# Performance work log

Hardware: AMD Instinct MI355X
Metric: run time of the kernel (lower is better)

Reference implementation:

```python
import jax, jax.numpy as jnp
import numpy as np

THRESHOLD = 0.5        # correspondence distance threshold (init kwarg)
MAX_ITERS = 50         # fixed iteration count (open3d's max_iteration)
EPS = 1e-6


def setup_inputs() -> dict:
    key = jax.random.key(0)
    k1, k2 = jax.random.split(key)
    B, N, M = 8, 2048, 2048
    source = jax.random.normal(k1, (B, N, 3), dtype=jnp.float32)
    target = jax.random.normal(k2, (B, M, 3), dtype=jnp.float32)
    return {"source": source, "target": target}


def _icp(source, target):
    """Batched point-to-point ICP. source: (B,N,3), target: (B,M,3) -> (B,4,4)."""
    B, N, _ = source.shape
    dt = source.dtype
    t_sq = jnp.sum(target * target, axis=-1)  # (B,M), constant across iterations

    def step(T, _):
        R, tr = T[:, :3, :3], T[:, :3, 3]
        src = jnp.einsum('bij,bnj->bni', R, source) + tr[:, None, :]  # (B,N,3)
        # brute-force nearest neighbor: squared distances (B,N,M)
        d2 = (jnp.sum(src * src, axis=-1)[:, :, None]
              - 2.0 * jnp.einsum('bnd,bmd->bnm', src, target)
              + t_sq[:, None, :])
        idx = jnp.argmin(d2, axis=-1)                                   # (B,N)
        mind2 = jnp.take_along_axis(d2, idx[..., None], axis=-1)[..., 0]
        nn = jnp.take_along_axis(target, idx[..., None], axis=1)        # (B,N,3)
        # inlier mask: correspondences within threshold
        w = (mind2 < THRESHOLD * THRESHOLD).astype(dt)                  # (B,N)
        wsum = jnp.maximum(jnp.sum(w, axis=-1, keepdims=True), EPS)     # (B,1)
        cs = jnp.sum(w[..., None] * src, axis=1) / wsum                 # (B,3)
        ct = jnp.sum(w[..., None] * nn, axis=1) / wsum                  # (B,3)
        Sc = src - cs[:, None, :]
        Tc = nn - ct[:, None, :]
        # cross-covariance H = sum_n w_n (s_n - cs)(t_n - ct)^T  -> (B,3,3)
        H = jnp.einsum('bn,bni,bnj->bij', w, Sc, Tc)
        U, _, Vh = jnp.linalg.svd(H, full_matrices=False)
        V = jnp.swapaxes(Vh, -1, -2)
        # reflection fix (Kabsch): R = V diag(1,1,sign(det(V U^T))) U^T
        d = jnp.sign(jnp.linalg.det(jnp.einsum('bij,bkj->bik', V, U)))
        scale = jnp.stack([jnp.ones_like(d), jnp.ones_like(d), d], axis=-1)
        Rd = jnp.einsum('bij,bj,bkj->bik', V, scale, U)                 # (B,3,3)
        td = ct - jnp.einsum('bij,bj->bi', Rd, cs)                      # (B,3)
        top = jnp.concatenate([Rd, td[:, :, None]], axis=-1)            # (B,3,4)
        bot = jnp.broadcast_to(jnp.array([0., 0., 0., 1.], dtype=dt), (B, 1, 4))
        delta = jnp.concatenate([top, bot], axis=1)                     # (B,4,4)
        return jnp.einsum('bij,bjk->bik', delta, T), None

    T0 = jnp.broadcast_to(jnp.eye(4, dtype=dt), (B, 4, 4))
    Tfin, _ = jax.lax.scan(step, T0, None, length=MAX_ITERS)
    return Tfin


def reference(source, target):
    return _icp(source, target)
```

## Files before the change

kernel.cpp:

```cpp
#include <hip/hip_runtime.h>
#include <stdint.h>

#define BATCH 8
#define NPTS 2048
#define MPTS 2048
#define ITERS 50
#define THR2 0.25f
#define CHUNKS 32
#define SRC_PER_BLOCK 64
#define PTS 8
#define NTHREADS 1024
#define NWAVES 16
#define SLICE_LEN 16

__global__ __launch_bounds__(NTHREADS)
void icp_kernel(const float* __restrict__ src,
                const float* __restrict__ tgt,
                float* __restrict__ out,
                float* __restrict__ ws)
{
    const int tid   = threadIdx.x;
    const int blk   = blockIdx.x;
    const int b     = blk >> 5;
    const int chunk = blk & 31;
    const int g     = tid & 7;
    const int s     = tid >> 3;
    const int lane  = tid & 63;
    const int wv    = tid >> 6;

    __shared__ float4 tgt4[MPTS];
    __shared__ float  red[NWAVES][65];
    __shared__ float  srcP[SRC_PER_BLOCK][3];
    __shared__ float4 bcastT4[3];

    const float* tb = tgt + (size_t)b * MPTS * 3;
    for (int m = tid; m < MPTS; m += NTHREADS) {
        float tx = tb[m*3+0], ty = tb[m*3+1], tz = tb[m*3+2];
        tgt4[m] = make_float4(-2.f*tx, -2.f*ty, -2.f*tz, tx*tx + ty*ty + tz*tz);
    }
    const float* sb = src + (size_t)b * NPTS * 3 + (size_t)chunk * SRC_PER_BLOCK * 3;
    if (tid < SRC_PER_BLOCK) {
        srcP[tid][0] = sb[tid*3+0];
        srcP[tid][1] = sb[tid*3+1];
        srcP[tid][2] = sb[tid*3+2];
    }
    float px[PTS], py[PTS], pz[PTS];
#pragma unroll
    for (int r = 0; r < PTS; ++r) {
        int i = g*PTS + r;
        px[r] = sb[i*3+0]; py[r] = sb[i*3+1]; pz[r] = sb[i*3+2];
    }
    __syncthreads();

    float r00=1.f,r01=0.f,r02=0.f, r10=0.f,r11=1.f,r12=0.f, r20=0.f,r21=0.f,r22=1.f;
    float t0=0.f,t1=0.f,t2=0.f;

    unsigned int* stamp = (unsigned int*)ws;
    float* slots = ws + 512;

    for (int it = 0; it < ITERS; ++it) {
        float sx[PTS], sy[PTS], sz[PTS];
#pragma unroll
        for (int r = 0; r < PTS; ++r) {
            sx[r] = r00*px[r] + r01*py[r] + r02*pz[r] + t0;
            sy[r] = r10*px[r] + r11*py[r] + r12*pz[r] + t1;
            sz[r] = r20*px[r] + r21*py[r] + r22*pz[r] + t2;
        }
        float best[PTS];
#pragma unroll
        for (int r = 0; r < PTS; ++r) best[r] = __int_as_float(0x7F800000);

        const int base = s * SLICE_LEN;
#pragma unroll 8
        for (int i = 0; i < SLICE_LEN; ++i) {
            int jo = (i + s) & (SLICE_LEN - 1);
            int jj = base + jo;
            float4 q = tgt4[jj];
#pragma unroll
            for (int r = 0; r < PTS; ++r) {
                float d = fmaf(sx[r], q.x, fmaf(sy[r], q.y, fmaf(sz[r], q.z, q.w)));
                unsigned int pd = (__float_as_uint(d) & 0xFFFFF800u) | (unsigned int)jj;
                best[r] = fminf(best[r], __uint_as_float(pd));
            }
        }
#pragma unroll
        for (int r = 0; r < PTS; ++r) {
            float v = best[r];
            v = fminf(v, __shfl_xor(v, 8, 64));
            v = fminf(v, __shfl_xor(v, 16, 64));
            v = fminf(v, __shfl_xor(v, 32, 64));
            best[r] = v;
        }
        if (lane < 8) {
#pragma unroll
            for (int r = 0; r < PTS; ++r) red[wv][lane*PTS + r] = best[r];
        }
        __syncthreads();

        if (tid < 64) {
            float m = red[0][tid];
#pragma unroll
            for (int ww = 1; ww < NWAVES; ++ww) m = fminf(m, red[ww][tid]);
            unsigned int mb = __float_as_uint(m);
            int   bi   = (int)(mb & 0x7FFu);
            float dmin = __uint_as_float(mb & 0xFFFFF800u);

            float ppx = srcP[tid][0], ppy = srcP[tid][1], ppz = srcP[tid][2];
            float qx = r00*ppx + r01*ppy + r02*ppz + t0;
            float qy = r10*ppx + r11*ppy + r12*ppz + t1;
            float qz = r20*ppx + r21*ppy + r22*ppz + t2;
            float s2 = qx*qx + qy*qy + qz*qz;
            float w = (dmin + s2 < THR2) ? 1.f : 0.f;
            float4 nnq = tgt4[bi];
            float nx = -0.5f*nnq.x, ny = -0.5f*nnq.y, nz = -0.5f*nnq.z;

            float v[16];
            v[0]=w;      v[1]=w*qx;    v[2]=w*qy;    v[3]=w*qz;
            v[4]=w*nx;   v[5]=w*ny;    v[6]=w*nz;
            v[7]=w*qx*nx;  v[8]=w*qx*ny;  v[9]=w*qx*nz;
            v[10]=w*qy*nx; v[11]=w*qy*ny; v[12]=w*qy*nz;
            v[13]=w*qz*nx; v[14]=w*qz*ny; v[15]=w*qz*nz;
#pragma unroll
            for (int j = 0; j < 16; ++j) {
                float a = v[j];
#pragma unroll
                for (int off = 1; off < 64; off <<= 1) a += __shfl_xor(a, off, 64);
                v[j] = a;
            }
            const unsigned int want = (unsigned int)(it + 1);
            const int sbase = ((it & 1) * BATCH + b) * CHUNKS;
            if (tid == 0) {
                float* sp = slots + (size_t)(sbase + chunk) * 16;
#pragma unroll
                for (int j = 0; j < 16; ++j)
                    __hip_atomic_store(&sp[j], v[j], __ATOMIC_RELAXED, __HIP_MEMORY_SCOPE_AGENT);
                asm volatile("s_waitcnt vmcnt(0)" ::: "memory");
                __hip_atomic_store(&stamp[sbase + chunk], want, __ATOMIC_RELAXED, __HIP_MEMORY_SCOPE_AGENT);
            }
            {
                const unsigned int* st = stamp + sbase;
                unsigned int sv;
                do {
                    sv = (lane < CHUNKS)
                         ? __hip_atomic_load(&st[lane], __ATOMIC_RELAXED, __HIP_MEMORY_SCOPE_AGENT)
                         : want;
                } while (!__all(sv == want));
                asm volatile("" ::: "memory");
            }
            float S_own = 0.f;
            if (tid < 16) {
                const float* gp = slots + (size_t)sbase * 16 + tid;
                float lv[CHUNKS];
#pragma unroll
                for (int c = 0; c < CHUNKS; ++c)
                    lv[c] = __hip_atomic_load(&gp[c*16], __ATOMIC_RELAXED, __HIP_MEMORY_SCOPE_AGENT);
#pragma unroll
                for (int c = 0; c < CHUNKS; ++c) S_own += lv[c];
            }
            float S[16];
#pragma unroll
            for (int j = 0; j < 16; ++j) S[j] = __shfl(S_own, j, 64);

            float wsum = fmaxf(S[0], 1e-6f);
            float inv  = 1.f / wsum;
            float ax=S[1], ay=S[2], az=S[3], bx=S[4], by=S[5], bz=S[6];
            float H00=S[7] -ax*bx*inv, H01=S[8] -ax*by*inv, H02=S[9] -ax*bz*inv;
            float H10=S[10]-ay*bx*inv, H11=S[11]-ay*by*inv, H12=S[12]-ay*bz*inv;
            float H20=S[13]-az*bx*inv, H21=S[14]-az*by*inv, H22=S[15]-az*bz*inv;

            float a00 = H00*H00 + H10*H10 + H20*H20;
            float a01 = H00*H01 + H10*H11 + H20*H21;
            float a02 = H00*H02 + H10*H12 + H20*H22;
            float a11 = H01*H01 + H11*H11 + H21*H21;
            float a12 = H01*H02 + H11*H12 + H21*H22;
            float a22 = H02*H02 + H12*H12 + H22*H22;

            float v00=1.f,v01=0.f,v02=0.f, v10=0.f,v11=1.f,v12=0.f, v20=0.f,v21=0.f,v22=1.f;

            auto rot = [](float &app, float &aqq, float &apq,
                          float &arp, float &arq,
                          float &vp0, float &vq0, float &vp1, float &vq1, float &vp2, float &vq2) {
                float q = apq;
                if (fabsf(q) > 1e-20f) {
                    float tau = (aqq - app) / (2.f * q);
                    float tt  = (tau >= 0.f ? 1.f : -1.f) / (fabsf(tau) + sqrtf(1.f + tau*tau));
                    float c   = 1.f / sqrtf(1.f + tt*tt);
                    float sn  = tt * c;
                    app -= tt * q;
                    aqq += tt * q;
                    apq = 0.f;
                    float x = arp, y = arq;
                    arp = c*x - sn*y;  arq = sn*x + c*y;
                    float u, w2;
                    u = vp0; w2 = vq0; vp0 = c*u - sn*w2; vq0 = sn*u + c*w2;
                    u = vp1; w2 = vq1; vp1 = c*u - sn*w2; vq1 = sn*u + c*w2;
                    u = vp2; w2 = vq2; vp2 = c*u - sn*w2; vq2 = sn*u + c*w2;
                }
            };
#pragma unroll
            for (int sw = 0; sw < 5; ++sw) {
                rot(a00, a11, a01, a02, a12, v00, v01, v10, v11, v20, v21);
                rot(a00, a22, a02, a01, a12, v00, v02, v10, v12, v20, v22);
                rot(a11, a22, a12, a01, a02, v01, v02, v11, v12, v21, v22);
            }
            {
                float tmp;
                if (a00 < a11) { tmp=a00;a00=a11;a11=tmp; tmp=v00;v00=v01;v01=tmp; tmp=v10;v10=v11;v11=tmp; tmp=v20;v20=v21;v21=tmp; }
                if (a00 < a22) { tmp=a00;a00=a22;a22=tmp; tmp=v00;v00=v02;v02=tmp; tmp=v10;v10=v12;v12=tmp; tmp=v20;v20=v22;v22=tmp; }
                if (a11 < a22) { tmp=a11;a11=a22;a22=tmp; tmp=v01;v01=v02;v02=tmp; tmp=v11;v11=v12;v12=tmp; tmp=v21;v21=v22;v22=tmp; }
            }

            float Rd00=1.f,Rd01=0.f,Rd02=0.f, Rd10=0.f,Rd11=1.f,Rd12=0.f, Rd20=0.f,Rd21=0.f,Rd22=1.f;
            {
                float u0x = H00*v00 + H01*v10 + H02*v20;
                float u0y = H10*v00 + H11*v10 + H12*v20;
                float u0z = H20*v00 + H21*v10 + H22*v20;
                float n0 = sqrtf(u0x*u0x + u0y*u0y + u0z*u0z);
                if (n0 > 1e-20f) {
                    float in0 = 1.f/n0; u0x*=in0; u0y*=in0; u0z*=in0;
                    float u1x = H00*v01 + H01*v11 + H02*v21;
                    float u1y = H10*v01 + H11*v11 + H12*v21;
                    float u1z = H20*v01 + H21*v11 + H22*v21;
                    float d01 = u0x*u1x + u0y*u1y + u0z*u1z;
                    u1x -= d01*u0x; u1y -= d01*u0y; u1z -= d01*u0z;
                    float n1 = sqrtf(u1x*u1x + u1y*u1y + u1z*u1z);
                    if (!(n1 > 1e-20f)) {
                        float fx = fabsf(u0x), fy = fabsf(u0y), fz = fabsf(u0z);
                        float ex=0.f, ey=0.f, ez=0.f;
                        if (fx <= fy && fx <= fz) ex = 1.f; else if (fy <= fz) ey = 1.f; else ez = 1.f;
                        u1x = u0y*ez - u0z*ey; u1y = u0z*ex - u0x*ez; u1z = u0x*ey - u0y*ex;
                        n1 = sqrtf(u1x*u1x + u1y*u1y + u1z*u1z);
                    }
                    float in1 = 1.f/n1; u1x*=in1; u1y*=in1; u1z*=in1;
                    float u2x = u0y*u1z - u0z*u1y;
                    float u2y = u0z*u1x - u0x*u1z;
                    float u2z = u0x*u1y - u0y*u1x;
                    float detV = v00*(v11*v22 - v12*v21) - v01*(v10*v22 - v12*v20) + v02*(v10*v21 - v11*v20);
                    float dsg = (detV >= 0.f) ? 1.f : -1.f;
                    Rd00 = v00*u0x + v01*u1x + dsg*v02*u2x;
                    Rd01 = v00*u0y + v01*u1y + dsg*v02*u2y;
                    Rd02 = v00*u0z + v01*u1z + dsg*v02*u2z;
                    Rd10 = v10*u0x + v11*u1x + dsg*v12*u2x;
                    Rd11 = v10*u0y + v11*u1y + dsg*v12*u2y;
                    Rd12 = v10*u0z + v11*u1z + dsg*v12*u2z;
                    Rd20 = v20*u0x + v21*u1x + dsg*v22*u2x;
                    Rd21 = v20*u0y + v21*u1y + dsg*v22*u2y;
                    Rd22 = v20*u0z + v21*u1z + dsg*v22*u2z;
                }
            }
            float csx = ax*inv, csy = ay*inv, csz = az*inv;
            float ctx = bx*inv, cty = by*inv, ctz = bz*inv;
            float tdx = ctx - (Rd00*csx + Rd01*csy + Rd02*csz);
            float tdy = cty - (Rd10*csx + Rd11*csy + Rd12*csz);
            float tdz = ctz - (Rd20*csx + Rd21*csy + Rd22*csz);

            float nr00 = Rd00*r00 + Rd01*r10 + Rd02*r20;
            float nr01 = Rd00*r01 + Rd01*r11 + Rd02*r21;
            float nr02 = Rd00*r02 + Rd01*r12 + Rd02*r22;
            float nr10 = Rd10*r00 + Rd11*r10 + Rd12*r20;
            float nr11 = Rd10*r01 + Rd11*r11 + Rd12*r21;
            float nr12 = Rd10*r02 + Rd11*r12 + Rd12*r22;
            float nr20 = Rd20*r00 + Rd21*r10 + Rd22*r20;
            float nr21 = Rd20*r01 + Rd21*r11 + Rd22*r21;
            float nr22 = Rd20*r02 + Rd21*r12 + Rd22*r22;
            float nt0 = Rd00*t0 + Rd01*t1 + Rd02*t2 + tdx;
            float nt1 = Rd10*t0 + Rd11*t1 + Rd12*t2 + tdy;
            float nt2 = Rd20*t0 + Rd21*t1 + Rd22*t2 + tdz;

            if (tid == 0) {
                bcastT4[0] = make_float4(nr00, nr01, nr02, nt0);
                bcastT4[1] = make_float4(nr10, nr11, nr12, nt1);
                bcastT4[2] = make_float4(nr20, nr21, nr22, nt2);
            }
        }
        __syncthreads();
        {
            float4 tA = bcastT4[0], tB = bcastT4[1], tC = bcastT4[2];
            r00=tA.x; r01=tA.y; r02=tA.z; t0=tA.w;
            r10=tB.x; r11=tB.y; r12=tB.z; t1=tB.w;
            r20=tC.x; r21=tC.y; r22=tC.z; t2=tC.w;
        }
    }

    if (chunk == 0 && tid == 0) {
        float* o = out + (size_t)b * 16;
        o[0]=r00;  o[1]=r01;  o[2]=r02;  o[3]=t0;
        o[4]=r10;  o[5]=r11;  o[6]=r12;  o[7]=t1;
        o[8]=r20;  o[9]=r21;  o[10]=r22; o[11]=t2;
        o[12]=0.f; o[13]=0.f; o[14]=0.f; o[15]=1.f;
    }
}

extern "C" void kernel_launch(void* const* d_in, const int* in_sizes, int n_in,
                              void* d_out, int out_size, void* d_ws, size_t ws_size,
                              hipStream_t stream) {
    const float* src = (const float*)d_in[0];
    const float* tgt = (const float*)d_in[1];
    float* out = (float*)d_out;
    float* ws  = (float*)d_ws;

    hipMemsetAsync(d_ws, 0, 2048, stream);

    void* args[] = { (void*)&src, (void*)&tgt, (void*)&out, (void*)&ws };
    hipLaunchCooperativeKernel((const void*)icp_kernel,
                               dim3(BATCH * CHUNKS), dim3(NTHREADS),
                               args, 0, stream);
}
```

Measured before the change: 570.4 us.

## Pair two batch items per block with 64 chunks and parallel per-batch tails

Each block now holds the target clouds of two batch items (b and b+4) in shared memory and handles 32 source points of each. The grid stays at 256 blocks but splits into 4 pairs of 64 chunks. The tail (reduction, stamp exchange, Kabsch solve) for the two items runs on two separate waves in parallel, and a single stamp per block covers both. The aim is to shorten the per-iteration serial tail and spread the distance work differently. In exchange, shared memory doubles, each sync wait involves 64 chunks, and the slot reads double.

```diff
diff --git a/kernel.cpp b/kernel.cpp
--- a/kernel.cpp
+++ b/kernel.cpp
@@ -2,18 +2,19 @@
 #include <stdint.h>
 
 #define BATCH 8
+#define PAIRS 4
 #define NPTS 2048
 #define MPTS 2048
 #define ITERS 50
 #define THR2 0.25f
-#define CHUNKS 32
-#define SRC_PER_BLOCK 64
+#define CHUNKS 64
+#define SRC_PER_BLOCK 32
 #define PTS 8
 #define NTHREADS 1024
 #define NWAVES 16
-#define SLICE_LEN 16
-
-__global__ __launch_bounds__(NTHREADS)
+#define SLICE_LEN 8
+
+__global__ __launch_bounds__(NTHREADS, 4)
 void icp_kernel(const float* __restrict__ src,
                 const float* __restrict__ tgt,
                 float* __restrict__ out,
@@ -21,61 +22,75 @@
 {
     const int tid   = threadIdx.x;
     const int blk   = blockIdx.x;
-    const int b     = blk >> 5;
-    const int chunk = blk & 31;
-    const int g     = tid & 7;
-    const int s     = tid >> 3;
+    const int pair  = blk >> 6;
+    const int chunk = blk & 63;
+    const int bA    = pair;
+    const int bB    = pair + 4;
+    const int g     = tid & 3;
+    const int s     = tid >> 2;
     const int lane  = tid & 63;
     const int wv    = tid >> 6;
-
-    __shared__ float4 tgt4[MPTS];
-    __shared__ float  red[NWAVES][65];
-    __shared__ float  srcP[SRC_PER_BLOCK][3];
-    __shared__ float4 bcastT4[3];
-
-    const float* tb = tgt + (size_t)b * MPTS * 3;
+    const int pl    = lane & 31;
+
+    __shared__ float4 tgt4[2][MPTS];
+    __shared__ float  red[2][NWAVES][33];
+    __shared__ float  srcP[2][SRC_PER_BLOCK][3];
+    __shared__ float4 bcastT4[2][3];
+
+    const float* tbA = tgt + (size_t)bA * MPTS * 3;
+    const float* tbB = tgt + (size_t)bB * MPTS * 3;
     for (int m = tid; m < MPTS; m += NTHREADS) {
-        float tx = tb[m*3+0], ty = tb[m*3+1], tz = tb[m*3+2];
-        tgt4[m] = make_float4(-2.f*tx, -2.f*ty, -2.f*tz, tx*tx + ty*ty + tz*tz);
+        float tx = tbA[m*3+0], ty = tbA[m*3+1], tz = tbA[m*3+2];
+        tgt4[0][m] = make_float4(-2.f*tx, -2.f*ty, -2.f*tz, tx*tx + ty*ty + tz*tz);
+        tx = tbB[m*3+0]; ty = tbB[m*3+1]; tz = tbB[m*3+2];
+        tgt4[1][m] = make_float4(-2.f*tx, -2.f*ty, -2.f*tz, tx*tx + ty*ty + tz*tz);
     }
-    const float* sb = src + (size_t)b * NPTS * 3 + (size_t)chunk * SRC_PER_BLOCK * 3;
+    const float* sbA = src + ((size_t)bA * NPTS + (size_t)chunk * SRC_PER_BLOCK) * 3;
+    const float* sbB = src + ((size_t)bB * NPTS + (size_t)chunk * SRC_PER_BLOCK) * 3;
     if (tid < SRC_PER_BLOCK) {
-        srcP[tid][0] = sb[tid*3+0];
-        srcP[tid][1] = sb[tid*3+1];
-        srcP[tid][2] = sb[tid*3+2];
-    }
-    float px[PTS], py[PTS], pz[PTS];
-#pragma unroll
-    for (int r = 0; r < PTS; ++r) {
-        int i = g*PTS + r;
-        px[r] = sb[i*3+0]; py[r] = sb[i*3+1]; pz[r] = sb[i*3+2];
+        srcP[0][tid][0] = sbA[tid*3+0];
+        srcP[0][tid][1] = sbA[tid*3+1];
+        srcP[0][tid][2] = sbA[tid*3+2];
+    } else if (tid < 2*SRC_PER_BLOCK) {
+        int t = tid - SRC_PER_BLOCK;
+        srcP[1][t][0] = sbB[t*3+0];
+        srcP[1][t][1] = sbB[t*3+1];
+        srcP[1][t][2] = sbB[t*3+2];
     }
     __syncthreads();
 
-    float r00=1.f,r01=0.f,r02=0.f, r10=0.f,r11=1.f,r12=0.f, r20=0.f,r21=0.f,r22=1.f;
-    float t0=0.f,t1=0.f,t2=0.f;
+    float Ar00=1.f,Ar01=0.f,Ar02=0.f, Ar10=0.f,Ar11=1.f,Ar12=0.f, Ar20=0.f,Ar21=0.f,Ar22=1.f;
+    float At0=0.f,At1=0.f,At2=0.f;
+    float Br00=1.f,Br01=0.f,Br02=0.f, Br10=0.f,Br11=1.f,Br12=0.f, Br20=0.f,Br21=0.f,Br22=1.f;
+    float Bt0=0.f,Bt1=0.f,Bt2=0.f;
 
     unsigned int* stamp = (unsigned int*)ws;
     float* slots = ws + 512;
 
-    for (int it = 0; it < ITERS; ++it) {
+    auto dist_phase = [&](int X,
+                          float r00, float r01, float r02,
+                          float r10, float r11, float r12,
+                          float r20, float r21, float r22,
+                          float t0, float t1, float t2) {
         float sx[PTS], sy[PTS], sz[PTS];
 #pragma unroll
         for (int r = 0; r < PTS; ++r) {
-            sx[r] = r00*px[r] + r01*py[r] + r02*pz[r] + t0;
-            sy[r] = r10*px[r] + r11*py[r] + r12*pz[r] + t1;
-            sz[r] = r20*px[r] + r21*py[r] + r22*pz[r] + t2;
+            int p = g*PTS + r;
+            float ppx = srcP[X][p][0], ppy = srcP[X][p][1], ppz = srcP[X][p][2];
+            sx[r] = r00*ppx + r01*ppy + r02*ppz + t0;
+            sy[r] = r10*ppx + r11*ppy + r12*ppz + t1;
+            sz[r] = r20*ppx + r21*ppy + r22*ppz + t2;
         }
         float best[PTS];
 #pragma unroll
         for (int r = 0; r < PTS; ++r) best[r] = __int_as_float(0x7F800000);
 
         const int base = s * SLICE_LEN;
-#pragma unroll 8
+#pragma unroll
         for (int i = 0; i < SLICE_LEN; ++i) {
             int jo = (i + s) & (SLICE_LEN - 1);
             int jj = base + jo;
-            float4 q = tgt4[jj];
+            float4 q = tgt4[X][jj];
 #pragma unroll
             for (int r = 0; r < PTS; ++r) {
                 float d = fmaf(sx[r], q.x, fmaf(sy[r], q.y, fmaf(sz[r], q.z, q.w)));
@@ -86,208 +101,246 @@
 #pragma unroll
         for (int r = 0; r < PTS; ++r) {
             float v = best[r];
+            v = fminf(v, __shfl_xor(v, 4, 64));
             v = fminf(v, __shfl_xor(v, 8, 64));
             v = fminf(v, __shfl_xor(v, 16, 64));
             v = fminf(v, __shfl_xor(v, 32, 64));
             best[r] = v;
         }
-        if (lane < 8) {
-#pragma unroll
-            for (int r = 0; r < PTS; ++r) red[wv][lane*PTS + r] = best[r];
-        }
+        if (lane < 4) {
+#pragma unroll
+            for (int r = 0; r < PTS; ++r) red[X][wv][lane*PTS + r] = best[r];
+        }
+    };
+
+    auto tail_pre = [&](int X, int it,
+                        float r00, float r01, float r02,
+                        float r10, float r11, float r12,
+                        float r20, float r21, float r22,
+                        float t0, float t1, float t2) {
+        float m = red[X][0][pl];
+#pragma unroll
+        for (int ww = 1; ww < NWAVES; ++ww) m = fminf(m, red[X][ww][pl]);
+        unsigned int mb = __float_as_uint(m);
+        int   bi   = (int)(mb & 0x7FFu);
+        float dmin = __uint_as_float(mb & 0xFFFFF800u);
+
+        float ppx = srcP[X][pl][0], ppy = srcP[X][pl][1], ppz = srcP[X][pl][2];
+        float qx = r00*ppx + r01*ppy + r02*ppz + t0;
+        float qy = r10*ppx + r11*ppy + r12*ppz + t1;
+        float qz = r20*ppx + r21*ppy + r22*ppz + t2;
+        float s2 = qx*qx + qy*qy + qz*qz;
+        float w = (dmin + s2 < THR2) ? 1.f : 0.f;
+        float4 nnq = tgt4[X][bi];
+        float nx = -0.5f*nnq.x, ny = -0.5f*nnq.y, nz = -0.5f*nnq.z;
+
+        float v[16];
+        v[0]=w;      v[1]=w*qx;    v[2]=w*qy;    v[3]=w*qz;
+        v[4]=w*nx;   v[5]=w*ny;    v[6]=w*nz;
+        v[7]=w*qx*nx;  v[8]=w*qx*ny;  v[9]=w*qx*nz;
+        v[10]=w*qy*nx; v[11]=w*qy*ny; v[12]=w*qy*nz;
+        v[13]=w*qz*nx; v[14]=w*qz*ny; v[15]=w*qz*nz;
+#pragma unroll
+        for (int j = 0; j < 16; ++j) {
+            float a = v[j];
+#pragma unroll
+            for (int off = 1; off < 32; off <<= 1) a += __shfl_xor(a, off, 64);
+            v[j] = a;
+        }
+        if (lane == 0) {
+            float* sp = slots + ((((size_t)(it & 1) * PAIRS + pair) * 2 + X) * CHUNKS + chunk) * 16;
+#pragma unroll
+            for (int j = 0; j < 16; ++j)
+                __hip_atomic_store(&sp[j], v[j], __ATOMIC_RELAXED, __HIP_MEMORY_SCOPE_AGENT);
+        }
+        asm volatile("s_waitcnt vmcnt(0)" ::: "memory");
+    };
+
+    auto tail_post = [&](int X, int it,
+                         float r00, float r01, float r02,
+                         float r10, float r11, float r12,
+                         float r20, float r21, float r22,
+                         float t0, float t1, float t2) {
+        const unsigned int want = (unsigned int)(it + 1);
+        const unsigned int* st = stamp + ((it & 1) * PAIRS + pair) * CHUNKS;
+        unsigned int sv;
+        do {
+            sv = __hip_atomic_load(&st[lane], __ATOMIC_RELAXED, __HIP_MEMORY_SCOPE_AGENT);
+        } while (!__all(sv >= want));
+        asm volatile("" ::: "memory");
+
+        float S_own = 0.f;
+        if (lane < 16) {
+            const float* gp = slots + ((((size_t)(it & 1) * PAIRS + pair) * 2 + X) * CHUNKS) * 16 + lane;
+            float lv[32];
+#pragma unroll
+            for (int c = 0; c < 32; ++c)
+                lv[c] = __hip_atomic_load(&gp[c*16], __ATOMIC_RELAXED, __HIP_MEMORY_SCOPE_AGENT);
+#pragma unroll
+            for (int c = 0; c < 32; ++c) S_own += lv[c];
+#pragma unroll
+            for (int c = 0; c < 32; ++c)
+                lv[c] = __hip_atomic_load(&gp[(32 + c)*16], __ATOMIC_RELAXED, __HIP_MEMORY_SCOPE_AGENT);
+#pragma unroll
+            for (int c = 0; c < 32; ++c) S_own += lv[c];
+        }
+        float S[16];
+#pragma unroll
+        for (int j = 0; j < 16; ++j) S[j] = __shfl(S_own, j, 64);
+
+        float wsum = fmaxf(S[0], 1e-6f);
+        float inv  = 1.f / wsum;
+        float ax=S[1], ay=S[2], az=S[3], bx=S[4], by=S[5], bz=S[6];
+        float H00=S[7] -ax*bx*inv, H01=S[8] -ax*by*inv, H02=S[9] -ax*bz*inv;
+        float H10=S[10]-ay*bx*inv, H11=S[11]-ay*by*inv, H12=S[12]-ay*bz*inv;
+        float H20=S[13]-az*bx*inv, H21=S[14]-az*by*inv, H22=S[15]-az*bz*inv;
+
+        float a00 = H00*H00 + H10*H10 + H20*H20;
+        float a01 = H00*H01 + H10*H11 + H20*H21;
+        float a02 = H00*H02 + H10*H12 + H20*H22;
+        float a11 = H01*H01 + H11*H11 + H21*H21;
+        float a12 = H01*H02 + H11*H12 + H21*H22;
+        float a22 = H02*H02 + H12*H12 + H22*H22;
+
+        float v00=1.f,v01=0.f,v02=0.f, v10=0.f,v11=1.f,v12=0.f, v20=0.f,v21=0.f,v22=1.f;
+
+        auto rot = [](float &app, float &aqq, float &apq,
+                      float &arp, float &arq,
+                      float &vp0, float &vq0, float &vp1, float &vq1, float &vp2, float &vq2) {
+            float q = apq;
+            if (fabsf(q) > 1e-20f) {
+                float tau = (aqq - app) / (2.f * q);
+                float tt  = (tau >= 0.f ? 1.f : -1.f) / (fabsf(tau) + sqrtf(1.f + tau*tau));
+                float c   = 1.f / sqrtf(1.f + tt*tt);
+                float sn  = tt * c;
+                app -= tt * q;
+                aqq += tt * q;
+                apq = 0.f;
+                float x = arp, y = arq;
+                arp = c*x - sn*y;  arq = sn*x + c*y;
+                float u, w2;
+                u = vp0; w2 = vq0; vp0 = c*u - sn*w2; vq0 = sn*u + c*w2;
+                u = vp1; w2 = vq1; vp1 = c*u - sn*w2; vq1 = sn*u + c*w2;
+                u = vp2; w2 = vq2; vp2 = c*u - sn*w2; vq2 = sn*u + c*w2;
+            }
+        };
+#pragma unroll
+        for (int sw = 0; sw < 5; ++sw) {
+            rot(a00, a11, a01, a02, a12, v00, v01, v10, v11, v20, v21);
+            rot(a00, a22, a02, a01, a12, v00, v02, v10, v12, v20, v22);
+            rot(a11, a22, a12, a01, a02, v01, v02, v11, v12, v21, v22);
+        }
+        {
+            float tmp;
+            if (a00 < a11) { tmp=a00;a00=a11;a11=tmp; tmp=v00;v00=v01;v01=tmp; tmp=v10;v10=v11;v11=tmp; tmp=v20;v20=v21;v21=tmp; }
+            if (a00 < a22) { tmp=a00;a00=a22;a22=tmp; tmp=v00;v00=v02;v02=tmp; tmp=v10;v10=v12;v12=tmp; tmp=v20;v20=v22;v22=tmp; }
+            if (a11 < a22) { tmp=a11;a11=a22;a22=tmp; tmp=v01;v01=v02;v02=tmp; tmp=v11;v11=v12;v12=tmp; tmp=v21;v21=v22;v22=tmp; }
+        }
+
+        float Rd00=1.f,Rd01=0.f,Rd02=0.f, Rd10=0.f,Rd11=1.f,Rd12=0.f, Rd20=0.f,Rd21=0.f,Rd22=1.f;
+        {
+            float u0x = H00*v00 + H01*v10 + H02*v20;
+            float u0y = H10*v00 + H11*v10 + H12*v20;
+            float u0z = H20*v00 + H21*v10 + H22*v20;
+            float n0 = sqrtf(u0x*u0x + u0y*u0y + u0z*u0z);
+            if (n0 > 1e-20f) {
+                float in0 = 1.f/n0; u0x*=in0; u0y*=in0; u0z*=in0;
+                float u1x = H00*v01 + H01*v11 + H02*v21;
+                float u1y = H10*v01 + H11*v11 + H12*v21;
+                float u1z = H20*v01 + H21*v11 + H22*v21;
+                float d01 = u0x*u1x + u0y*u1y + u0z*u1z;
+                u1x -= d01*u0x; u1y -= d01*u0y; u1z -= d01*u0z;
+                float n1 = sqrtf(u1x*u1x + u1y*u1y + u1z*u1z);
+                if (!(n1 > 1e-20f)) {
+                    float fx = fabsf(u0x), fy = fabsf(u0y), fz = fabsf(u0z);
+                    float ex=0.f, ey=0.f, ez=0.f;
+                    if (fx <= fy && fx <= fz) ex = 1.f; else if (fy <= fz) ey = 1.f; else ez = 1.f;
+                    u1x = u0y*ez - u0z*ey; u1y = u0z*ex - u0x*ez; u1z = u0x*ey - u0y*ex;
+                    n1 = sqrtf(u1x*u1x + u1y*u1y + u1z*u1z);
+                }
+                float in1 = 1.f/n1; u1x*=in1; u1y*=in1; u1z*=in1;
+                float u2x = u0y*u1z - u0z*u1y;
+                float u2y = u0z*u1x - u0x*u1z;
+                float u2z = u0x*u1y - u0y*u1x;
+                float detV = v00*(v11*v22 - v12*v21) - v01*(v10*v22 - v12*v20) + v02*(v10*v21 - v11*v20);
+                float dsg = (detV >= 0.f) ? 1.f : -1.f;
+                Rd00 = v00*u0x + v01*u1x + dsg*v02*u2x;
+                Rd01 = v00*u0y + v01*u1y + dsg*v02*u2y;
+                Rd02 = v00*u0z + v01*u1z + dsg*v02*u2z;
+                Rd10 = v10*u0x + v11*u1x + dsg*v12*u2x;
+                Rd11 = v10*u0y + v11*u1y + dsg*v12*u2y;
+                Rd12 = v10*u0z + v11*u1z + dsg*v12*u2z;
+                Rd20 = v20*u0x + v21*u1x + dsg*v22*u2x;
+                Rd21 = v20*u0y + v21*u1y + dsg*v22*u2y;
+                Rd22 = v20*u0z + v21*u1z + dsg*v22*u2z;
+            }
+        }
+        float csx = ax*inv, csy = ay*inv, csz = az*inv;
+        float ctx = bx*inv, cty = by*inv, ctz = bz*inv;
+        float tdx = ctx - (Rd00*csx + Rd01*csy + Rd02*csz);
+        float tdy = cty - (Rd10*csx + Rd11*csy + Rd12*csz);
+        float tdz = ctz - (Rd20*csx + Rd21*csy + Rd22*csz);
+
+        float nr00 = Rd00*r00 + Rd01*r10 + Rd02*r20;
+        float nr01 = Rd00*r01 + Rd01*r11 + Rd02*r21;
+        float nr02 = Rd00*r02 + Rd01*r12 + Rd02*r22;
+        float nr10 = Rd10*r00 + Rd11*r10 + Rd12*r20;
+        float nr11 = Rd10*r01 + Rd11*r11 + Rd12*r21;
+        float nr12 = Rd10*r02 + Rd11*r12 + Rd12*r22;
+        float nr20 = Rd20*r00 + Rd21*r10 + Rd22*r20;
+        float nr21 = Rd20*r01 + Rd21*r11 + Rd22*r21;
+        float nr22 = Rd20*r02 + Rd21*r12 + Rd22*r22;
+        float nt0 = Rd00*t0 + Rd01*t1 + Rd02*t2 + tdx;
+        float nt1 = Rd10*t0 + Rd11*t1 + Rd12*t2 + tdy;
+        float nt2 = Rd20*t0 + Rd21*t1 + Rd22*t2 + tdz;
+
+        if (lane == 0) {
+            bcastT4[X][0] = make_float4(nr00, nr01, nr02, nt0);
+            bcastT4[X][1] = make_float4(nr10, nr11, nr12, nt1);
+            bcastT4[X][2] = make_float4(nr20, nr21, nr22, nt2);
+        }
+    };
+
+    for (int it = 0; it < ITERS; ++it) {
+        dist_phase(0, Ar00,Ar01,Ar02, Ar10,Ar11,Ar12, Ar20,Ar21,Ar22, At0,At1,At2);
+        dist_phase(1, Br00,Br01,Br02, Br10,Br11,Br12, Br20,Br21,Br22, Bt0,Bt1,Bt2);
         __syncthreads();
 
-        if (tid < 64) {
-            float m = red[0][tid];
-#pragma unroll
-            for (int ww = 1; ww < NWAVES; ++ww) m = fminf(m, red[ww][tid]);
-            unsigned int mb = __float_as_uint(m);
-            int   bi   = (int)(mb & 0x7FFu);
-            float dmin = __uint_as_float(mb & 0xFFFFF800u);
-
-            float ppx = srcP[tid][0], ppy = srcP[tid][1], ppz = srcP[tid][2];
-            float qx = r00*ppx + r01*ppy + r02*ppz + t0;
-            float qy = r10*ppx + r11*ppy + r12*ppz + t1;
-            float qz = r20*ppx + r21*ppy + r22*ppz + t2;
-            float s2 = qx*qx + qy*qy + qz*qz;
-            float w = (dmin + s2 < THR2) ? 1.f : 0.f;
-            float4 nnq = tgt4[bi];
-            float nx = -0.5f*nnq.x, ny = -0.5f*nnq.y, nz = -0.5f*nnq.z;
-
-            float v[16];
-            v[0]=w;      v[1]=w*qx;    v[2]=w*qy;    v[3]=w*qz;
-            v[4]=w*nx;   v[5]=w*ny;    v[6]=w*nz;
-            v[7]=w*qx*nx;  v[8]=w*qx*ny;  v[9]=w*qx*nz;
-            v[10]=w*qy*nx; v[11]=w*qy*ny; v[12]=w*qy*nz;
-            v[13]=w*qz*nx; v[14]=w*qz*ny; v[15]=w*qz*nz;
-#pragma unroll
-            for (int j = 0; j < 16; ++j) {
-                float a = v[j];
-#pragma unroll
-                for (int off = 1; off < 64; off <<= 1) a += __shfl_xor(a, off, 64);
-                v[j] = a;
-            }
-            const unsigned int want = (unsigned int)(it + 1);
-            const int sbase = ((it & 1) * BATCH + b) * CHUNKS;
-            if (tid == 0) {
-                float* sp = slots + (size_t)(sbase + chunk) * 16;
-#pragma unroll
-                for (int j = 0; j < 16; ++j)
-                    __hip_atomic_store(&sp[j], v[j], __ATOMIC_RELAXED, __HIP_MEMORY_SCOPE_AGENT);
-                asm volatile("s_waitcnt vmcnt(0)" ::: "memory");
-                __hip_atomic_store(&stamp[sbase + chunk], want, __ATOMIC_RELAXED, __HIP_MEMORY_SCOPE_AGENT);
-            }
-            {
-                const unsigned int* st = stamp + sbase;
-                unsigned int sv;
-                do {
-                    sv = (lane < CHUNKS)
-                         ? __hip_atomic_load(&st[lane], __ATOMIC_RELAXED, __HIP_MEMORY_SCOPE_AGENT)
-                         : want;
-                } while (!__all(sv == want));
-                asm volatile("" ::: "memory");
-            }
-            float S_own = 0.f;
-            if (tid < 16) {
-                const float* gp = slots + (size_t)sbase * 16 + tid;
-                float lv[CHUNKS];
-#pragma unroll
-                for (int c = 0; c < CHUNKS; ++c)
-                    lv[c] = __hip_atomic_load(&gp[c*16], __ATOMIC_RELAXED, __HIP_MEMORY_SCOPE_AGENT);
-#pragma unroll
-                for (int c = 0; c < CHUNKS; ++c) S_own += lv[c];
-            }
-            float S[16];
-#pragma unroll
-            for (int j = 0; j < 16; ++j) S[j] = __shfl(S_own, j, 64);
-
-            float wsum = fmaxf(S[0], 1e-6f);
-            float inv  = 1.f / wsum;
-            float ax=S[1], ay=S[2], az=S[3], bx=S[4], by=S[5], bz=S[6];
-            float H00=S[7] -ax*bx*inv, H01=S[8] -ax*by*inv, H02=S[9] -ax*bz*inv;
-            float H10=S[10]-ay*bx*inv, H11=S[11]-ay*by*inv, H12=S[12]-ay*bz*inv;
-            float H20=S[13]-az*bx*inv, H21=S[14]-az*by*inv, H22=S[15]-az*bz*inv;
-
-            float a00 = H00*H00 + H10*H10 + H20*H20;
-            float a01 = H00*H01 + H10*H11 + H20*H21;
-            float a02 = H00*H02 + H10*H12 + H20*H22;
-            float a11 = H01*H01 + H11*H11 + H21*H21;
-            float a12 = H01*H02 + H11*H12 + H21*H22;
-            float a22 = H02*H02 + H12*H12 + H22*H22;
-
-            float v00=1.f,v01=0.f,v02=0.f, v10=0.f,v11=1.f,v12=0.f, v20=0.f,v21=0.f,v22=1.f;
-
-            auto rot = [](float &app, float &aqq, float &apq,
-                          float &arp, float &arq,
-                          float &vp0, float &vq0, float &vp1, float &vq1, float &vp2, float &vq2) {
-                float q = apq;
-                if (fabsf(q) > 1e-20f) {
-                    float tau = (aqq - app) / (2.f * q);
-                    float tt  = (tau >= 0.f ? 1.f : -1.f) / (fabsf(tau) + sqrtf(1.f + tau*tau));
-                    float c   = 1.f / sqrtf(1.f + tt*tt);
-                    float sn  = tt * c;
-                    app -= tt * q;
-                    aqq += tt * q;
-                    apq = 0.f;
-                    float x = arp, y = arq;
-                    arp = c*x - sn*y;  arq = sn*x + c*y;
-                    float u, w2;
-                    u = vp0; w2 = vq0; vp0 = c*u - sn*w2; vq0 = sn*u + c*w2;
-                    u = vp1; w2 = vq1; vp1 = c*u - sn*w2; vq1 = sn*u + c*w2;
-                    u = vp2; w2 = vq2; vp2 = c*u - sn*w2; vq2 = sn*u + c*w2;
-                }
-            };
-#pragma unroll
-            for (int sw = 0; sw < 5; ++sw) {
-                rot(a00, a11, a01, a02, a12, v00, v01, v10, v11, v20, v21);
-                rot(a00, a22, a02, a01, a12, v00, v02, v10, v12, v20, v22);
-                rot(a11, a22, a12, a01, a02, v01, v02, v11, v12, v21, v22);
-            }
-            {
-                float tmp;
-                if (a00 < a11) { tmp=a00;a00=a11;a11=tmp; tmp=v00;v00=v01;v01=tmp; tmp=v10;v10=v11;v11=tmp; tmp=v20;v20=v21;v21=tmp; }
-                if (a00 < a22) { tmp=a00;a00=a22;a22=tmp; tmp=v00;v00=v02;v02=tmp; tmp=v10;v10=v12;v12=tmp; tmp=v20;v20=v22;v22=tmp; }
-                if (a11 < a22) { tmp=a11;a11=a22;a22=tmp; tmp=v01;v01=v02;v02=tmp; tmp=v11;v11=v12;v12=tmp; tmp=v21;v21=v22;v22=tmp; }
-            }
-
-            float Rd00=1.f,Rd01=0.f,Rd02=0.f, Rd10=0.f,Rd11=1.f,Rd12=0.f, Rd20=0.f,Rd21=0.f,Rd22=1.f;
-            {
-                float u0x = H00*v00 + H01*v10 + H02*v20;
-                float u0y = H10*v00 + H11*v10 + H12*v20;
-                float u0z = H20*v00 + H21*v10 + H22*v20;
-                float n0 = sqrtf(u0x*u0x + u0y*u0y + u0z*u0z);
-                if (n0 > 1e-20f) {
-                    float in0 = 1.f/n0; u0x*=in0; u0y*=in0; u0z*=in0;
-                    float u1x = H00*v01 + H01*v11 + H02*v21;
-                    float u1y = H10*v01 + H11*v11 + H12*v21;
-                    float u1z = H20*v01 + H21*v11 + H22*v21;
-                    float d01 = u0x*u1x + u0y*u1y + u0z*u1z;
-                    u1x -= d01*u0x; u1y -= d01*u0y; u1z -= d01*u0z;
-                    float n1 = sqrtf(u1x*u1x + u1y*u1y + u1z*u1z);
-                    if (!(n1 > 1e-20f)) {
-                        float fx = fabsf(u0x), fy = fabsf(u0y), fz = fabsf(u0z);
-                        float ex=0.f, ey=0.f, ez=0.f;
-                        if (fx <= fy && fx <= fz) ex = 1.f; else if (fy <= fz) ey = 1.f; else ez = 1.f;
-                        u1x = u0y*ez - u0z*ey; u1y = u0z*ex - u0x*ez; u1z = u0x*ey - u0y*ex;
-                        n1 = sqrtf(u1x*u1x + u1y*u1y + u1z*u1z);
-                    }
-                    float in1 = 1.f/n1; u1x*=in1; u1y*=in1; u1z*=in1;
-                    float u2x = u0y*u1z - u0z*u1y;
-                    float u2y = u0z*u1x - u0x*u1z;
-                    float u2z = u0x*u1y - u0y*u1x;
-                    float detV = v00*(v11*v22 - v12*v21) - v01*(v10*v22 - v12*v20) + v02*(v10*v21 - v11*v20);
-                    float dsg = (detV >= 0.f) ? 1.f : -1.f;
-                    Rd00 = v00*u0x + v01*u1x + dsg*v02*u2x;
-                    Rd01 = v00*u0y + v01*u1y + dsg*v02*u2y;
-                    Rd02 = v00*u0z + v01*u1z + dsg*v02*u2z;
-                    Rd10 = v10*u0x + v11*u1x + dsg*v12*u2x;
-                    Rd11 = v10*u0y + v11*u1y + dsg*v12*u2y;
-                    Rd12 = v10*u0z + v11*u1z + dsg*v12*u2z;
-                    Rd20 = v20*u0x + v21*u1x + dsg*v22*u2x;
-                    Rd21 = v20*u0y + v21*u1y + dsg*v22*u2y;
-                    Rd22 = v20*u0z + v21*u1z + dsg*v22*u2z;
-                }
-            }
-            float csx = ax*inv, csy = ay*inv, csz = az*inv;
-            float ctx = bx*inv, cty = by*inv, ctz = bz*inv;
-            float tdx = ctx - (Rd00*csx + Rd01*csy + Rd02*csz);
-            float tdy = cty - (Rd10*csx + Rd11*csy + Rd12*csz);
-            float tdz = ctz - (Rd20*csx + Rd21*csy + Rd22*csz);
-
-            float nr00 = Rd00*r00 + Rd01*r10 + Rd02*r20;
-            float nr01 = Rd00*r01 + Rd01*r11 + Rd02*r21;
-            float nr02 = Rd00*r02 + Rd01*r12 + Rd02*r22;
-            float nr10 = Rd10*r00 + Rd11*r10 + Rd12*r20;
-            float nr11 = Rd10*r01 + Rd11*r11 + Rd12*r21;
-            float nr12 = Rd10*r02 + Rd11*r12 + Rd12*r22;
-            float nr20 = Rd20*r00 + Rd21*r10 + Rd22*r20;
-            float nr21 = Rd20*r01 + Rd21*r11 + Rd22*r21;
-            float nr22 = Rd20*r02 + Rd21*r12 + Rd22*r22;
-            float nt0 = Rd00*t0 + Rd01*t1 + Rd02*t2 + tdx;
-            float nt1 = Rd10*t0 + Rd11*t1 + Rd12*t2 + tdy;
-            float nt2 = Rd20*t0 + Rd21*t1 + Rd22*t2 + tdz;
-
-            if (tid == 0) {
-                bcastT4[0] = make_float4(nr00, nr01, nr02, nt0);
-                bcastT4[1] = make_float4(nr10, nr11, nr12, nt1);
-                bcastT4[2] = make_float4(nr20, nr21, nr22, nt2);
-            }
-        }
+        if (wv == 0)      tail_pre(0, it, Ar00,Ar01,Ar02, Ar10,Ar11,Ar12, Ar20,Ar21,Ar22, At0,At1,At2);
+        else if (wv == 1) tail_pre(1, it, Br00,Br01,Br02, Br10,Br11,Br12, Br20,Br21,Br22, Bt0,Bt1,Bt2);
         __syncthreads();
+
+        if (tid == 0) {
+            __hip_atomic_store(&stamp[((it & 1) * PAIRS + pair) * CHUNKS + chunk],
+                               (unsigned int)(it + 1), __ATOMIC_RELAXED, __HIP_MEMORY_SCOPE_AGENT);
+        }
+        if (wv == 0)      tail_post(0, it, Ar00,Ar01,Ar02, Ar10,Ar11,Ar12, Ar20,Ar21,Ar22, At0,At1,At2);
+        else if (wv == 1) tail_post(1, it, Br00,Br01,Br02, Br10,Br11,Br12, Br20,Br21,Br22, Bt0,Bt1,Bt2);
+        __syncthreads();
+
         {
-            float4 tA = bcastT4[0], tB = bcastT4[1], tC = bcastT4[2];
-            r00=tA.x; r01=tA.y; r02=tA.z; t0=tA.w;
-            r10=tB.x; r11=tB.y; r12=tB.z; t1=tB.w;
-            r20=tC.x; r21=tC.y; r22=tC.z; t2=tC.w;
+            float4 tA = bcastT4[0][0], tBr = bcastT4[0][1], tC = bcastT4[0][2];
+            Ar00=tA.x; Ar01=tA.y; Ar02=tA.z; At0=tA.w;
+            Ar10=tBr.x; Ar11=tBr.y; Ar12=tBr.z; At1=tBr.w;
+            Ar20=tC.x; Ar21=tC.y; Ar22=tC.z; At2=tC.w;
+            float4 uA = bcastT4[1][0], uB = bcastT4[1][1], uC = bcastT4[1][2];
+            Br00=uA.x; Br01=uA.y; Br02=uA.z; Bt0=uA.w;
+            Br10=uB.x; Br11=uB.y; Br12=uB.z; Bt1=uB.w;
+            Br20=uC.x; Br21=uC.y; Br22=uC.z; Bt2=uC.w;
         }
     }
 
     if (chunk == 0 && tid == 0) {
-        float* o = out + (size_t)b * 16;
-        o[0]=r00;  o[1]=r01;  o[2]=r02;  o[3]=t0;
-        o[4]=r10;  o[5]=r11;  o[6]=r12;  o[7]=t1;
-        o[8]=r20;  o[9]=r21;  o[10]=r22; o[11]=t2;
-        o[12]=0.f; o[13]=0.f; o[14]=0.f; o[15]=1.f;
+        float* oA = out + (size_t)bA * 16;
+        oA[0]=Ar00;  oA[1]=Ar01;  oA[2]=Ar02;  oA[3]=At0;
+        oA[4]=Ar10;  oA[5]=Ar11;  oA[6]=Ar12;  oA[7]=At1;
+        oA[8]=Ar20;  oA[9]=Ar21;  oA[10]=Ar22; oA[11]=At2;
+        oA[12]=0.f;  oA[13]=0.f;  oA[14]=0.f;  oA[15]=1.f;
+        float* oB = out + (size_t)bB * 16;
+        oB[0]=Br00;  oB[1]=Br01;  oB[2]=Br02;  oB[3]=Bt0;
+        oB[4]=Br10;  oB[5]=Br11;  oB[6]=Br12;  oB[7]=Bt1;
+        oB[8]=Br20;  oB[9]=Br21;  oB[10]=Br22; oB[11]=Bt2;
+        oB[12]=0.f;  oB[13]=0.f;  oB[14]=0.f;  oB[15]=1.f;
     }
 }
 
@@ -303,6 +356,6 @@
 
     void* args[] = { (void*)&src, (void*)&tgt, (void*)&out, (void*)&ws };
     hipLaunchCooperativeKernel((const void*)icp_kernel,
-                               dim3(BATCH * CHUNKS), dim3(NTHREADS),
+                               dim3(PAIRS * CHUNKS), dim3(NTHREADS),
                                args, 0, stream);
 }
```

Result: slower. 734.7 us (+28.8%).
